# Kernel optimization log

Hardware: AMD Instinct MI355X
Metric: run time of the kernel (lower is better)

Reference implementation:

```python
import jax, jax.numpy as jnp
import numpy as np
from jax import lax

B, D, C, K = 8192, 512, 1000, 8
EPS = 1e-8
TEMP = 0.2
NEG = -10000.0


def setup_inputs() -> dict:
    key = jax.random.key(0)
    ks = jax.random.split(key, 6)
    z = jax.random.normal(ks[0], (B, D), dtype=jnp.float32)
    n_exp = jax.random.randint(ks[1], (B,), 0, K, dtype=jnp.int32)
    s1 = 1.0 / np.sqrt(D)
    W1 = jax.random.normal(ks[2], (K, D, D), dtype=jnp.float32) * s1
    b1 = jax.random.normal(ks[3], (K, D), dtype=jnp.float32) * 0.01
    W2 = jax.random.normal(ks[4], (K, D, C), dtype=jnp.float32) * s1
    b2 = jax.random.normal(ks[5], (K, C), dtype=jnp.float32) * 0.01
    return {"z": z, "n_exp": n_exp, "W1": W1, "b1": b1, "W2": W2, "b2": b2}


def _gates_one(p, c, n):
    # p: [K,C] softmax probs for one sample; c: [K] confidences; n: scalar int
    pn = p / (jnp.linalg.norm(p, axis=-1, keepdims=True) + EPS)
    S = pn @ pn.T  # [K,K] pairwise cosine similarity
    sel0 = jnp.zeros((K,), dtype=bool).at[jnp.argmax(c)].set(True)

    def body(t, sel):
        # max cosine sim of each candidate to already-selected set
        max_sim = jnp.max(jnp.where(sel[None, :], S, -jnp.inf), axis=1)
        dist = jnp.where(sel, -jnp.inf, 1.0 - max_sim)
        new = sel.at[jnp.argmax(dist)].set(True)
        return jnp.where(t < n, new, sel)

    sel = lax.fori_loop(1, K, body, sel0)
    gate_logits = jnp.where(sel, c, NEG) / TEMP
    return jax.nn.softmax(gate_logits)


def reference(z, n_exp, W1, b1, W2, b2):
    # K expert MLPs, batched: [B,d] -> [B,K,C]
    h = jax.nn.relu(jnp.einsum('bd,kde->bke', z, W1) + b1[None])
    logits_all = jnp.einsum('bke,kec->bkc', h, W2) + b2[None]
    probs = jax.nn.softmax(logits_all, axis=-1)
    conf = jnp.max(probs, axis=-1)  # [B,K]
    gates = jax.vmap(_gates_one)(probs, conf, n_exp)  # [B,K]
    logits = jnp.einsum('bkc,bk->bc', logits_all, gates)
    return logits, gates
```

## Files before the change

kernel.cpp:

```cpp
#include <hip/hip_runtime.h>
#include <math.h>

#define B_SZ 8192
#define D_DIM 512
#define C_DIM 1000
#define C_PAD 1024
#define K_EXP 8
#define TEMP_INV 5.0f
#define EPS_N 1e-8f

typedef __attribute__((ext_vector_type(8))) short frag_ab;
typedef __attribute__((ext_vector_type(4))) float frag_cd;

__device__ __forceinline__ short f2bf(float f) {
    unsigned u = __builtin_bit_cast(unsigned, f);
    unsigned r = (u + 0x7fffu + ((u >> 16) & 1u)) >> 16;
    return (short)r;
}
__device__ __forceinline__ float bf2f(short s) {
    unsigned u = ((unsigned)(unsigned short)s) << 16;
    return __builtin_bit_cast(float, u);
}
__device__ __forceinline__ void split2(float v, short& s0, short& s1) {
    s0 = f2bf(v);
    s1 = f2bf(v - bf2f(s0));
}

__device__ __forceinline__ void gl_lds16(const short* g, short* l) {
    __builtin_amdgcn_global_load_lds(
        (const __attribute__((address_space(1))) unsigned int*)(const void*)g,
        (__attribute__((address_space(3))) unsigned int*)(void*)l,
        16, 0, 0);
}

__global__ __launch_bounds__(256) void prep_z(const float* __restrict__ z,
                                              short* __restrict__ p0, short* __restrict__ p1) {
    int idx = blockIdx.x * 256 + threadIdx.x;
    float v = z[idx];
    short a, b; split2(v, a, b);
    p0[idx] = a; p1[idx] = b;
}

__global__ __launch_bounds__(256) void prep_w1(const float* __restrict__ W1,
                                               short* __restrict__ p0, short* __restrict__ p1) {
    int idx = blockIdx.x * 256 + threadIdx.x;
    int k = idx >> 18;
    int e = (idx >> 9) & 511;
    int d = idx & 511;
    float v = W1[((size_t)k << 18) + (size_t)d * 512 + e];
    short a, b; split2(v, a, b);
    p0[idx] = a; p1[idx] = b;
}

__global__ __launch_bounds__(256) void prep_w2(const float* __restrict__ W2,
                                               short* __restrict__ p0, short* __restrict__ p1) {
    int idx = blockIdx.x * 256 + threadIdx.x;
    int k = idx >> 19;
    int c = (idx >> 9) & 1023;
    int e = idx & 511;
    float v = (c < C_DIM) ? W2[(size_t)k * (D_DIM * C_DIM) + (size_t)e * C_DIM + c] : 0.f;
    short a, b; split2(v, a, b);
    p0[idx] = a; p1[idx] = b;
}

__global__ __launch_bounds__(256, 4) void gemm_split(
    const short* __restrict__ A0, const short* __restrict__ A1, long long aBatch,
    const short* __restrict__ B0, const short* __restrict__ B1, long long bBatch,
    const float* __restrict__ bias, int biasBatch,
    float* __restrict__ Cf, long long cBatch, int ldc, int Nout,
    short* __restrict__ H0, short* __restrict__ H1, long long hBatch,
    int mt, int nt, int mode)
{
    const int lin = blockIdx.x;
    const int k = lin & 7;
    const int rem = lin >> 3;
    const int gm = (mt >= 4) ? 4 : mt;
    const int win = rem / (gm * nt);
    const int local = rem % (gm * nt);
    const int m0 = (win * gm + local / nt) * 128;
    const int n0 = (local % nt) * 128;

    const int tid = threadIdx.x;
    const int lane = tid & 63;
    const int wv = tid >> 6;
    const int wm = (wv & 1) * 64;
    const int wn = (wv >> 1) * 64;

    __shared__ short lds[16384];

    const short* gA0 = A0 + (size_t)k * aBatch + (size_t)m0 * 512;
    const short* gA1 = A1 + (size_t)k * aBatch + (size_t)m0 * 512;
    const short* gB0 = B0 + (size_t)k * bBatch + (size_t)n0 * 512;
    const short* gB1 = B1 + (size_t)k * bBatch + (size_t)n0 * 512;
    short* ldsA = lds;
    short* ldsB = lds + 8192;

    frag_cd acc[4][4];
#pragma unroll
    for (int i = 0; i < 4; i++)
#pragma unroll
        for (int j = 0; j < 4; j++)
            acc[i][j] = (frag_cd){0.f, 0.f, 0.f, 0.f};

    const int srow = tid >> 2;
    const int sch  = (tid & 3) * 8;

    for (int k0 = 0; k0 < 512; k0 += 32) {
        const short* ga[2] = {gA0, gA1};
        const short* gb[2] = {gB0, gB1};
#pragma unroll
        for (int p = 0; p < 2; p++) {
#pragma unroll
            for (int hh = 0; hh < 2; hh++) {
                int row = hh * 64 + srow;
                gl_lds16(ga[p] + (size_t)row * 512 + k0 + sch,
                         ldsA + p * 4096 + row * 32 + sch);
                gl_lds16(gb[p] + (size_t)row * 512 + k0 + sch,
                         ldsB + p * 4096 + row * 32 + sch);
            }
        }
        __syncthreads();

        frag_ab af[2][4], bfr[2][4];
#pragma unroll
        for (int p = 0; p < 2; p++)
#pragma unroll
            for (int t = 0; t < 4; t++) {
                af[p][t]  = *(const frag_ab*)(ldsA + p * 4096 + (wm + t * 16 + (lane & 15)) * 32 + (lane >> 4) * 8);
                bfr[p][t] = *(const frag_ab*)(ldsB + p * 4096 + (wn + t * 16 + (lane & 15)) * 32 + (lane >> 4) * 8);
            }

#pragma unroll
        for (int i = 0; i < 4; i++)
#pragma unroll
            for (int j = 0; j < 4; j++) {
                frag_cd c = acc[i][j];
                c = __builtin_amdgcn_mfma_f32_16x16x32_bf16(af[0][i], bfr[0][j], c, 0, 0, 0);
                c = __builtin_amdgcn_mfma_f32_16x16x32_bf16(af[0][i], bfr[1][j], c, 0, 0, 0);
                c = __builtin_amdgcn_mfma_f32_16x16x32_bf16(af[1][i], bfr[0][j], c, 0, 0, 0);
                acc[i][j] = c;
            }
        __syncthreads();
    }

    const int r0 = (lane >> 4) * 4;
    const int cc = lane & 15;
    if (mode == 0) {
        float* C = Cf + (size_t)k * cBatch;
        const float* bb = bias + (size_t)k * biasBatch;
#pragma unroll
        for (int i = 0; i < 4; i++) {
            int rowb = m0 + wm + i * 16 + r0;
#pragma unroll
            for (int j = 0; j < 4; j++) {
                int col = n0 + wn + j * 16 + cc;
                if (col < Nout) {
                    float b = bb[col];
#pragma unroll
                    for (int r = 0; r < 4; r++)
                        C[(size_t)(rowb + r) * ldc + col] = acc[i][j][r] + b;
                }
            }
        }
    } else {
        short* h0 = H0 + (size_t)k * hBatch;
        short* h1 = H1 + (size_t)k * hBatch;
        const float* bb = bias + (size_t)k * biasBatch;
#pragma unroll
        for (int i = 0; i < 4; i++) {
            int rowb = m0 + wm + i * 16 + r0;
#pragma unroll
            for (int j = 0; j < 4; j++) {
                int col = n0 + wn + j * 16 + cc;
                float b = bb[col];
#pragma unroll
                for (int r = 0; r < 4; r++) {
                    float v = fmaxf(acc[i][j][r] + b, 0.f);
                    short s0, s1; split2(v, s0, s1);
                    size_t o = (size_t)(rowb + r) * 512 + col;
                    h0[o] = s0; h1[o] = s1;
                }
            }
        }
    }
}

__global__ __launch_bounds__(256) void gate_combine(
    const float* __restrict__ L,
    const int* __restrict__ n_exp,
    float* __restrict__ out_logits,
    float* __restrict__ out_gates,
    int Bc)
{
    const int wv = threadIdx.x >> 6;
    const int lane = threadIdx.x & 63;
    const int b = blockIdx.x * 4 + wv;
    const size_t kcs = (size_t)Bc * C_DIM;
    const float* Lb = L + (size_t)b * C_DIM;

    __shared__ float Sm[4][64];
    __shared__ float Zm[4][8];

    float mx[K_EXP], Zs[K_EXP], dd[36];
#pragma unroll
    for (int k = 0; k < K_EXP; k++) { mx[k] = -INFINITY; Zs[k] = 0.f; }
#pragma unroll
    for (int p = 0; p < 36; p++) dd[p] = 0.f;

    for (int c = lane; c < C_DIM; c += 64) {
        float e[K_EXP];
#pragma unroll
        for (int k = 0; k < K_EXP; k++) {
            float l = Lb[(size_t)k * kcs + c];
            mx[k] = fmaxf(mx[k], l);
            e[k] = __expf(l);
            Zs[k] += e[k];
        }
        int idx = 0;
#pragma unroll
        for (int i = 0; i < K_EXP; i++)
#pragma unroll
            for (int j = i; j < K_EXP; j++) {
                dd[idx] = fmaf(e[i], e[j], dd[idx]);
                idx++;
            }
    }

#pragma unroll
    for (int off = 32; off > 0; off >>= 1) {
#pragma unroll
        for (int k = 0; k < K_EXP; k++) {
            mx[k] = fmaxf(mx[k], __shfl_xor(mx[k], off, 64));
            Zs[k] += __shfl_xor(Zs[k], off, 64);
        }
#pragma unroll
        for (int p = 0; p < 36; p++)
            dd[p] += __shfl_xor(dd[p], off, 64);
    }

    if (lane == 0) {
        int idx = 0;
#pragma unroll
        for (int i = 0; i < K_EXP; i++)
#pragma unroll
            for (int j = i; j < K_EXP; j++) {
                Sm[wv][i * 8 + j] = dd[idx];
                Sm[wv][j * 8 + i] = dd[idx];
                idx++;
            }
#pragma unroll
        for (int k = 0; k < K_EXP; k++) Zm[wv][k] = Zs[k];
    }

    const int ti = lane >> 3, tj = lane & 7;
    const float Zi = Zm[wv][ti], Zj = Zm[wv][tj];
    const float dij = Sm[wv][ti * 8 + tj];
    const float dii = Sm[wv][ti * 8 + ti];
    const float djj = Sm[wv][tj * 8 + tj];
    const float ni = sqrtf(dii) / Zi + EPS_N;
    const float nj = sqrtf(djj) / Zj + EPS_N;
    const float cosij = (dij / (Zi * Zj)) / (ni * nj);

    float conf[K_EXP];
#pragma unroll
    for (int k = 0; k < K_EXP; k++) conf[k] = __expf(mx[k]) / Zs[k];

    int i0 = 0; float bcf = conf[0];
#pragma unroll
    for (int k = 1; k < K_EXP; k++)
        if (conf[k] > bcf) { bcf = conf[k]; i0 = k; }
    unsigned sel = 1u << i0;
    const int n = n_exp[b];

    for (int t = 1; t < K_EXP; t++) {
        float v = ((sel >> tj) & 1u) ? cosij : -INFINITY;
        v = fmaxf(v, __shfl_xor(v, 1, 64));
        v = fmaxf(v, __shfl_xor(v, 2, 64));
        v = fmaxf(v, __shfl_xor(v, 4, 64));
        float dist = ((sel >> ti) & 1u) ? -INFINITY : 1.0f - v;
        float bv = dist; int bi = ti;
#pragma unroll
        for (int off = 8; off < 64; off <<= 1) {
            float ov = __shfl_xor(bv, off, 64);
            int oi = __shfl_xor(bi, off, 64);
            if (ov > bv || (ov == bv && oi < bi)) { bv = ov; bi = oi; }
        }
        if (t < n) sel |= 1u << bi;
    }

    float cmax = -INFINITY;
#pragma unroll
    for (int k = 0; k < K_EXP; k++)
        if ((sel >> k) & 1u) cmax = fmaxf(cmax, conf[k]);
    float g[K_EXP], gsum = 0.f;
#pragma unroll
    for (int k = 0; k < K_EXP; k++) {
        g[k] = ((sel >> k) & 1u) ? __expf((conf[k] - cmax) * TEMP_INV) : 0.f;
        gsum += g[k];
    }
    const float ginv = 1.0f / gsum;
#pragma unroll
    for (int k = 0; k < K_EXP; k++) g[k] *= ginv;

    if (lane == 0) {
        float4* og = (float4*)(out_gates + (size_t)b * K_EXP);
        og[0] = make_float4(g[0], g[1], g[2], g[3]);
        og[1] = make_float4(g[4], g[5], g[6], g[7]);
    }

    for (int c = lane; c < C_DIM; c += 64) {
        float o = 0.f;
#pragma unroll
        for (int k = 0; k < K_EXP; k++)
            o = fmaf(g[k], Lb[(size_t)k * kcs + c], o);
        out_logits[(size_t)b * C_DIM + c] = o;
    }
}

extern "C" void kernel_launch(void* const* d_in, const int* in_sizes, int n_in,
                              void* d_out, int out_size, void* d_ws, size_t ws_size,
                              hipStream_t stream) {
    const float* z     = (const float*)d_in[0];
    const int*   n_exp = (const int*)d_in[1];
    const float* W1    = (const float*)d_in[2];
    const float* b1    = (const float*)d_in[3];
    const float* W2    = (const float*)d_in[4];
    const float* b2    = (const float*)d_in[5];
    float* out_logits = (float*)d_out;
    float* out_gates  = (float*)d_out + (size_t)B_SZ * C_DIM;

    const size_t zP   = (size_t)B_SZ * D_DIM * 2;
    const size_t w1P  = (size_t)K_EXP * D_DIM * D_DIM * 2;
    const size_t w2P  = (size_t)K_EXP * C_PAD * D_DIM * 2;
    const size_t fixedBytes = 2 * (zP + w1P + w2P);

    int nch = 1;
    while (nch < 32 && fixedBytes + (size_t)(B_SZ / nch) * 48384 > ws_size) nch *= 2;
    const int Bc = B_SZ / nch;

    char* w = (char*)d_ws;
    short* zp[2];  zp[0]  = (short*)w; zp[1]  = (short*)(w + zP);  w += 2 * zP;
    short* w1t[2]; w1t[0] = (short*)w; w1t[1] = (short*)(w + w1P); w += 2 * w1P;
    short* w2t[2]; w2t[0] = (short*)w; w2t[1] = (short*)(w + w2P); w += 2 * w2P;
    const size_t hP = (size_t)K_EXP * Bc * D_DIM * 2;
    short* hp[2];  hp[0]  = (short*)w; hp[1]  = (short*)(w + hP);  w += 2 * hP;
    float* Lb = (float*)w;

    prep_z <<<dim3((B_SZ * D_DIM) / 256), 256, 0, stream>>>(z, zp[0], zp[1]);
    prep_w1<<<dim3((K_EXP * D_DIM * D_DIM) / 256), 256, 0, stream>>>(W1, w1t[0], w1t[1]);
    prep_w2<<<dim3((K_EXP * C_PAD * D_DIM) / 256), 256, 0, stream>>>(W2, w2t[0], w2t[1]);

    const int mt = Bc / 128;

    for (int ch = 0; ch < nch; ch++) {
        const int off = ch * Bc;
        const long long zoff = (long long)off * D_DIM;

        gemm_split<<<dim3(8 * mt * 4), 256, 0, stream>>>(
            zp[0] + zoff, zp[1] + zoff, 0LL,
            w1t[0], w1t[1], (long long)D_DIM * D_DIM,
            b1, D_DIM,
            nullptr, 0LL, 0, D_DIM,
            hp[0], hp[1], (long long)Bc * D_DIM,
            mt, 4, 1);

        gemm_split<<<dim3(8 * mt * 8), 256, 0, stream>>>(
            hp[0], hp[1], (long long)Bc * D_DIM,
            w2t[0], w2t[1], (long long)C_PAD * D_DIM,
            b2, C_DIM,
            Lb, (long long)Bc * C_DIM, C_DIM, C_DIM,
            nullptr, nullptr, 0LL,
            mt, 8, 0);

        gate_combine<<<dim3(Bc / 4), 256, 0, stream>>>(
            Lb, n_exp + off,
            out_logits + (size_t)off * C_DIM,
            out_gates + (size_t)off * K_EXP,
            Bc);
    }
}
```

Before: 538.1 us.

## Double-buffer GEMM LDS staging and tile-transpose weight prep kernels

```diff
diff --git a/kernel.cpp b/kernel.cpp
--- a/kernel.cpp
+++ b/kernel.cpp
@@ -41,29 +41,58 @@
     p0[idx] = a; p1[idx] = b;
 }
 
-__global__ __launch_bounds__(256) void prep_w1(const float* __restrict__ W1,
-                                               short* __restrict__ p0, short* __restrict__ p1) {
-    int idx = blockIdx.x * 256 + threadIdx.x;
-    int k = idx >> 18;
-    int e = (idx >> 9) & 511;
-    int d = idx & 511;
-    float v = W1[((size_t)k << 18) + (size_t)d * 512 + e];
-    short a, b; split2(v, a, b);
-    p0[idx] = a; p1[idx] = b;
-}
-
-__global__ __launch_bounds__(256) void prep_w2(const float* __restrict__ W2,
-                                               short* __restrict__ p0, short* __restrict__ p1) {
-    int idx = blockIdx.x * 256 + threadIdx.x;
-    int k = idx >> 19;
-    int c = (idx >> 9) & 1023;
-    int e = idx & 511;
-    float v = (c < C_DIM) ? W2[(size_t)k * (D_DIM * C_DIM) + (size_t)e * C_DIM + c] : 0.f;
-    short a, b; split2(v, a, b);
-    p0[idx] = a; p1[idx] = b;
-}
-
-__global__ __launch_bounds__(256, 4) void gemm_split(
+__global__ __launch_bounds__(256) void prep_w1t(const float* __restrict__ W1,
+                                                short* __restrict__ p0, short* __restrict__ p1) {
+    __shared__ float t[32][33];
+    const int k = blockIdx.z;
+    const int d0 = blockIdx.x * 32;
+    const int e0 = blockIdx.y * 32;
+    const int tx = threadIdx.x & 31, ty = threadIdx.x >> 5;
+    const float* src = W1 + ((size_t)k << 18);
+#pragma unroll
+    for (int r = 0; r < 4; r++) {
+        int d = d0 + ty + 8 * r;
+        t[ty + 8 * r][tx] = src[(size_t)d * 512 + e0 + tx];
+    }
+    __syncthreads();
+#pragma unroll
+    for (int r = 0; r < 4; r++) {
+        int e = e0 + ty + 8 * r;
+        int d = d0 + tx;
+        float v = t[tx][ty + 8 * r];
+        short a, b; split2(v, a, b);
+        size_t o = ((size_t)k << 18) + (size_t)e * 512 + d;
+        p0[o] = a; p1[o] = b;
+    }
+}
+
+__global__ __launch_bounds__(256) void prep_w2t(const float* __restrict__ W2,
+                                                short* __restrict__ p0, short* __restrict__ p1) {
+    __shared__ float t[32][33];
+    const int k = blockIdx.z;
+    const int e0 = blockIdx.x * 32;
+    const int c0 = blockIdx.y * 32;
+    const int tx = threadIdx.x & 31, ty = threadIdx.x >> 5;
+    const float* src = W2 + (size_t)k * (D_DIM * C_DIM);
+#pragma unroll
+    for (int r = 0; r < 4; r++) {
+        int e = e0 + ty + 8 * r;
+        int c = c0 + tx;
+        t[ty + 8 * r][tx] = (c < C_DIM) ? src[(size_t)e * C_DIM + c] : 0.f;
+    }
+    __syncthreads();
+#pragma unroll
+    for (int r = 0; r < 4; r++) {
+        int c = c0 + ty + 8 * r;
+        int e = e0 + tx;
+        float v = t[tx][ty + 8 * r];
+        short a, b; split2(v, a, b);
+        size_t o = (size_t)k * (C_PAD * D_DIM) + (size_t)c * 512 + e;
+        p0[o] = a; p1[o] = b;
+    }
+}
+
+__global__ __launch_bounds__(256, 2) void gemm_split(
     const short* __restrict__ A0, const short* __restrict__ A1, long long aBatch,
     const short* __restrict__ B0, const short* __restrict__ B1, long long bBatch,
     const float* __restrict__ bias, int biasBatch,
@@ -86,14 +115,12 @@
     const int wm = (wv & 1) * 64;
     const int wn = (wv >> 1) * 64;
 
-    __shared__ short lds[16384];
+    __shared__ short lds[32768];
 
     const short* gA0 = A0 + (size_t)k * aBatch + (size_t)m0 * 512;
     const short* gA1 = A1 + (size_t)k * aBatch + (size_t)m0 * 512;
     const short* gB0 = B0 + (size_t)k * bBatch + (size_t)n0 * 512;
     const short* gB1 = B1 + (size_t)k * bBatch + (size_t)n0 * 512;
-    short* ldsA = lds;
-    short* ldsB = lds + 8192;
 
     frag_cd acc[4][4];
 #pragma unroll
@@ -105,22 +132,31 @@
     const int srow = tid >> 2;
     const int sch  = (tid & 3) * 8;
 
-    for (int k0 = 0; k0 < 512; k0 += 32) {
+    auto stage = [&](int k0, short* buf) {
+        short* bA = buf;
+        short* bB = buf + 8192;
         const short* ga[2] = {gA0, gA1};
         const short* gb[2] = {gB0, gB1};
 #pragma unroll
-        for (int p = 0; p < 2; p++) {
+        for (int p = 0; p < 2; p++)
 #pragma unroll
             for (int hh = 0; hh < 2; hh++) {
                 int row = hh * 64 + srow;
-                gl_lds16(ga[p] + (size_t)row * 512 + k0 + sch,
-                         ldsA + p * 4096 + row * 32 + sch);
-                gl_lds16(gb[p] + (size_t)row * 512 + k0 + sch,
-                         ldsB + p * 4096 + row * 32 + sch);
-            }
-        }
+                gl_lds16(ga[p] + (size_t)row * 512 + k0 + sch, bA + p * 4096 + row * 32 + sch);
+                gl_lds16(gb[p] + (size_t)row * 512 + k0 + sch, bB + p * 4096 + row * 32 + sch);
+            }
+    };
+
+    stage(0, lds);
+
+    for (int it = 0; it < 16; it++) {
+        short* curb = lds + (it & 1) * 16384;
+        short* nxtb = lds + ((it + 1) & 1) * 16384;
         __syncthreads();
-
+        if (it + 1 < 16) stage((it + 1) * 32, nxtb);
+
+        short* ldsA = curb;
+        short* ldsB = curb + 8192;
         frag_ab af[2][4], bfr[2][4];
 #pragma unroll
         for (int p = 0; p < 2; p++)
@@ -140,7 +176,6 @@
                 c = __builtin_amdgcn_mfma_f32_16x16x32_bf16(af[1][i], bfr[0][j], c, 0, 0, 0);
                 acc[i][j] = c;
             }
-        __syncthreads();
     }
 
     const int r0 = (lane >> 4) * 4;
@@ -347,8 +382,8 @@
     float* Lb = (float*)w;
 
     prep_z <<<dim3((B_SZ * D_DIM) / 256), 256, 0, stream>>>(z, zp[0], zp[1]);
-    prep_w1<<<dim3((K_EXP * D_DIM * D_DIM) / 256), 256, 0, stream>>>(W1, w1t[0], w1t[1]);
-    prep_w2<<<dim3((K_EXP * C_PAD * D_DIM) / 256), 256, 0, stream>>>(W2, w2t[0], w2t[1]);
+    prep_w1t<<<dim3(16, 16, K_EXP), 256, 0, stream>>>(W1, w1t[0], w1t[1]);
+    prep_w2t<<<dim3(16, 32, K_EXP), 256, 0, stream>>>(W2, w2t[0], w2t[1]);
 
     const int mt = Bc / 128;
 
```

Result: faster. 516.6 us (-4.0%).
